# Performance work log

Hardware: AMD Instinct MI355X
Metric: run time of the kernel (lower is better)

## Reference

```python
import jax, jax.numpy as jnp
import numpy as np

# M = batch16 * (128^2+64^2+32^2+16^2+8^2) FPN pixels for 1024x1024 inputs, strides 8..128
M = 349184
C = 80          # num_classes
N_POS = 2048    # positive center locations

ALPHA = 0.25        # hm_focal_alpha
BETA = 4.0          # hm_focal_beta
GAMMA = 2.0         # loss_gamma
SIGMOID_CLAMP = 1e-4
POS_W = 1.0
NEG_W = 1.0
REG_W = 2.0         # reg_weight


def setup_inputs() -> dict:
    key = jax.random.key(0)
    k1, k2, k3, k4, k5, k6 = jax.random.split(key, 6)
    return {
        'logits_pred': jax.random.normal(k1, (M, C), jnp.float32),
        'flattened_hms': jax.random.uniform(k2, (M, C), jnp.float32),
        'reg_pred': jax.random.uniform(k3, (M, 4), jnp.float32),
        'reg_targets': jax.random.normal(k4, (M, 4), jnp.float32),
        'pos_inds': jax.random.randint(k5, (N_POS,), 0, M),
        'labels': jax.random.randint(k6, (N_POS,), 0, C),
    }


def _giou_loss(pred, target):
    # pred/target: [M,4] ltrb distances from grid point to box edges
    pl, pt, pr, pb = pred[:, 0], pred[:, 1], pred[:, 2], pred[:, 3]
    tl, tt, tr, tb = target[:, 0], target[:, 1], target[:, 2], target[:, 3]
    target_area = (tl + tr) * (tt + tb)
    pred_area = (pl + pr) * (pt + pb)
    w_intersect = jnp.minimum(pl, tl) + jnp.minimum(pr, tr)
    h_intersect = jnp.minimum(pb, tb) + jnp.minimum(pt, tt)
    g_w = jnp.maximum(pl, tl) + jnp.maximum(pr, tr)
    g_h = jnp.maximum(pb, tb) + jnp.maximum(pt, tt)
    ac_union = g_w * g_h
    area_intersect = w_intersect * h_intersect
    area_union = target_area + pred_area - area_intersect
    ious = (area_intersect + 1.0) / (area_union + 1.0)
    gious = ious - (ac_union - area_union) / (ac_union + 1e-7)
    return 1.0 - gious  # per-pixel giou loss


def reference(logits_pred, flattened_hms, reg_pred, reg_targets, pos_inds, labels):
    # ---- heatmap focal loss (CenterNet2 heatmap_focal_loss) ----
    pred = jnp.clip(jax.nn.sigmoid(logits_pred), SIGMOID_CLAMP, 1.0 - SIGMOID_CLAMP)
    neg_weights = (1.0 - flattened_hms) ** BETA  # zero at exact positives
    pos_pred = pred[pos_inds, labels]            # irregular gather, [N]
    pos_loss = jnp.log(pos_pred) * (1.0 - pos_pred) ** GAMMA
    neg_loss = jnp.log(1.0 - pred) * pred ** GAMMA * neg_weights
    pos_loss = -ALPHA * jnp.sum(pos_loss)
    neg_loss = -(1.0 - ALPHA) * jnp.sum(neg_loss)
    num_pos_avg = float(max(N_POS, 1))
    pos_loss = POS_W * pos_loss / num_pos_avg
    neg_loss = NEG_W * neg_loss / num_pos_avg

    valid = jnp.max(reg_targets, axis=1) >= 0  # [M] bool, replaces nonzero-gather
    # not_norm_reg=True -> per-location weight 1 on valid rows
    w = valid.astype(reg_pred.dtype)
    safe_targets = jnp.where(valid[:, None], reg_targets, 1.0)
    per_px = _giou_loss(reg_pred, safe_targets)
    reg_norm = jnp.maximum(jnp.sum(w), 1.0)
    reg_loss = REG_W * jnp.sum(per_px * w) / reg_norm

    return jnp.stack([pos_loss, neg_loss, reg_loss])
```

## Files before the change

### kernel.cpp

```cpp
#include <hip/hip_runtime.h>
#include <math.h>

#define M_ROWS   349184
#define C_CH     80
#define NPOS     2048
#define ALPHA    0.25f
#define SIG_CLMP 1.0e-4f
#define REG_W    2.0f

#define NBLOCKS  512
#define NTHREADS 1024
#define N4       6983680
#define CHUNK4   13640
#define ROWS_PB  682
#define POS_PB   4

typedef float vf4 __attribute__((ext_vector_type(4)));

__device__ __forceinline__ float fast_rcp(float x) {
    return __builtin_amdgcn_rcpf(x);
}

__device__ __forceinline__ float clamped_sigmoid(float x) {
    float p = fast_rcp(1.0f + __expf(-x));
    return fminf(fmaxf(p, SIG_CLMP), 1.0f - SIG_CLMP);
}

__device__ __forceinline__ float neg_term(float x, float h) {
    float p = clamped_sigmoid(x);
    float q = 1.0f - h;
    float q2 = q * q;
    return __logf(1.0f - p) * (p * p) * (q2 * q2);
}

__device__ __forceinline__ float neg_term4(vf4 x, vf4 h) {
    return neg_term(x.x, h.x) + neg_term(x.y, h.y) +
           neg_term(x.z, h.z) + neg_term(x.w, h.w);
}

__device__ __forceinline__ vf4 ldnt4(const vf4* p) {
    return __builtin_nontemporal_load(p);
}

__global__ __launch_bounds__(NTHREADS) void centernet_loss_main(
    const float* __restrict__ logits,
    const float* __restrict__ hms,
    const float* __restrict__ reg_pred,
    const float* __restrict__ reg_tgt,
    const int*   __restrict__ pos_inds,
    const int*   __restrict__ labels,
    float4* __restrict__ partials)
{
    const int t = threadIdx.x;
    const int b = ((int)blockIdx.x & 255) * 2 + ((int)blockIdx.x >> 8);

    float neg = 0.0f, giou = 0.0f, wsum = 0.0f, pos = 0.0f;

    const vf4* lg4 = (const vf4*)logits;
    const vf4* hm4 = (const vf4*)hms;

    const int start = b * CHUNK4;
    const int end   = start + CHUNK4;

    int i = start + t;
    for (; i + 5 * NTHREADS < end; i += 6 * NTHREADS) {
        vf4 x0 = ldnt4(&lg4[i]);
        vf4 x1 = ldnt4(&lg4[i + NTHREADS]);
        vf4 x2 = ldnt4(&lg4[i + 2 * NTHREADS]);
        vf4 x3 = ldnt4(&lg4[i + 3 * NTHREADS]);
        vf4 x4 = ldnt4(&lg4[i + 4 * NTHREADS]);
        vf4 x5 = ldnt4(&lg4[i + 5 * NTHREADS]);
        vf4 h0 = ldnt4(&hm4[i]);
        vf4 h1 = ldnt4(&hm4[i + NTHREADS]);
        vf4 h2 = ldnt4(&hm4[i + 2 * NTHREADS]);
        vf4 h3 = ldnt4(&hm4[i + 3 * NTHREADS]);
        vf4 h4 = ldnt4(&hm4[i + 4 * NTHREADS]);
        vf4 h5 = ldnt4(&hm4[i + 5 * NTHREADS]);
        neg += neg_term4(x0, h0);
        neg += neg_term4(x1, h1);
        neg += neg_term4(x2, h2);
        neg += neg_term4(x3, h3);
        neg += neg_term4(x4, h4);
        neg += neg_term4(x5, h5);
    }
    for (; i < end; i += NTHREADS) {
        neg += neg_term4(ldnt4(&lg4[i]), ldnt4(&hm4[i]));
    }

    const int rstart = b * ROWS_PB;
    const vf4* rp4 = (const vf4*)reg_pred;
    const vf4* rt4 = (const vf4*)reg_tgt;
    for (int r = rstart + t; r < rstart + ROWS_PB; r += NTHREADS) {
        vf4 tt = rt4[r];
        float mx = fmaxf(fmaxf(tt.x, tt.y), fmaxf(tt.z, tt.w));
        if (mx >= 0.0f) {
            vf4 p = rp4[r];
            float target_area = (tt.x + tt.z) * (tt.y + tt.w);
            float pred_area   = (p.x + p.z) * (p.y + p.w);
            float w_int = fminf(p.x, tt.x) + fminf(p.z, tt.z);
            float h_int = fminf(p.w, tt.w) + fminf(p.y, tt.y);
            float g_w   = fmaxf(p.x, tt.x) + fmaxf(p.z, tt.z);
            float g_h   = fmaxf(p.w, tt.w) + fmaxf(p.y, tt.y);
            float ac    = g_w * g_h;
            float ai    = w_int * h_int;
            float au    = target_area + pred_area - ai;
            float ious  = (ai + 1.0f) * fast_rcp(au + 1.0f);
            float gious = ious - (ac - au) * fast_rcp(ac + 1e-7f);
            giou += 1.0f - gious;
            wsum += 1.0f;
        }
    }

    if (t < POS_PB) {
        int k = b * POS_PB + t;
        int idx = pos_inds[k] * C_CH + labels[k];
        float p  = clamped_sigmoid(logits[idx]);
        float om = 1.0f - p;
        pos = __logf(p) * om * om;
    }

    const int lane = t & 63;
    const int wave = t >> 6;
    #pragma unroll
    for (int off = 32; off > 0; off >>= 1) {
        neg  += __shfl_down(neg,  off);
        giou += __shfl_down(giou, off);
        wsum += __shfl_down(wsum, off);
        pos  += __shfl_down(pos,  off);
    }
    __shared__ float smem[16][4];
    if (lane == 0) {
        smem[wave][0] = neg;  smem[wave][1] = giou;
        smem[wave][2] = wsum; smem[wave][3] = pos;
    }
    __syncthreads();
    if (t == 0) {
        float4 v = make_float4(0.f, 0.f, 0.f, 0.f);
        #pragma unroll
        for (int w = 0; w < 16; ++w) {
            v.x += smem[w][0]; v.y += smem[w][1];
            v.z += smem[w][2]; v.w += smem[w][3];
        }
        partials[blockIdx.x] = v;
    }
}

__global__ __launch_bounds__(256) void centernet_loss_reduce(
    const float4* __restrict__ partials,
    float* __restrict__ out)
{
    float neg = 0.0f, giou = 0.0f, wsum = 0.0f, pos = 0.0f;
    for (int i = threadIdx.x; i < NBLOCKS; i += 256) {
        float4 v = partials[i];
        neg += v.x; giou += v.y; wsum += v.z; pos += v.w;
    }
    const int lane = threadIdx.x & 63;
    const int wave = threadIdx.x >> 6;
    #pragma unroll
    for (int off = 32; off > 0; off >>= 1) {
        neg  += __shfl_down(neg,  off);
        giou += __shfl_down(giou, off);
        wsum += __shfl_down(wsum, off);
        pos  += __shfl_down(pos,  off);
    }
    __shared__ float smem[4][4];
    if (lane == 0) {
        smem[wave][0] = neg;  smem[wave][1] = giou;
        smem[wave][2] = wsum; smem[wave][3] = pos;
    }
    __syncthreads();
    if (threadIdx.x == 0) {
        float n = smem[0][0] + smem[1][0] + smem[2][0] + smem[3][0];
        float g = smem[0][1] + smem[1][1] + smem[2][1] + smem[3][1];
        float w = smem[0][2] + smem[1][2] + smem[2][2] + smem[3][2];
        float p = smem[0][3] + smem[1][3] + smem[2][3] + smem[3][3];
        const float inv_npos = 1.0f / (float)NPOS;
        out[0] = -ALPHA * p * inv_npos;
        out[1] = -(1.0f - ALPHA) * n * inv_npos;
        out[2] = REG_W * g / fmaxf(w, 1.0f);
    }
}

extern "C" void kernel_launch(void* const* d_in, const int* in_sizes, int n_in,
                              void* d_out, int out_size, void* d_ws, size_t ws_size,
                              hipStream_t stream) {
    const float* logits   = (const float*)d_in[0];
    const float* hms      = (const float*)d_in[1];
    const float* reg_pred = (const float*)d_in[2];
    const float* reg_tgt  = (const float*)d_in[3];
    const int*   pos_inds = (const int*)d_in[4];
    const int*   labels   = (const int*)d_in[5];
    float* out = (float*)d_out;
    float4* partials = (float4*)d_ws;

    centernet_loss_main<<<NBLOCKS, NTHREADS, 0, stream>>>(
        logits, hms, reg_pred, reg_tgt, pos_inds, labels, partials);
    centernet_loss_reduce<<<1, 256, 0, stream>>>(partials, out);
}
```

Before: 234.1 us.

## Drop sigmoid clamp via softplus form, retune grid, use plain loads

Computes the negative focal term as -softplus(x)*sigmoid(x)^2 (and the positive term as -softplus(-x)*(1-p)^2), removing the sigmoid clamp and the divide-then-log path. Doubles the block count with half the threads per block, adds an occupancy hint to launch bounds, and swaps nontemporal loads for ordinary loads issued in interleaved logits/heatmap order. Removing the clamp changes results slightly for extreme logits, and __expf(x) can overflow for large positive x, though the logits are standard normal. The kernel is memory-bound, so the arithmetic savings may not matter much.

```diff
diff --git a/kernel.cpp b/kernel.cpp
--- a/kernel.cpp
+++ b/kernel.cpp
@@ -5,15 +5,14 @@
 #define C_CH     80
 #define NPOS     2048
 #define ALPHA    0.25f
-#define SIG_CLMP 1.0e-4f
 #define REG_W    2.0f
 
-#define NBLOCKS  512
-#define NTHREADS 1024
+#define NBLOCKS  1024
+#define NTHREADS 512
 #define N4       6983680
-#define CHUNK4   13640
-#define ROWS_PB  682
-#define POS_PB   4
+#define CHUNK4   6820
+#define ROWS_PB  341
+#define POS_PB   2
 
 typedef float vf4 __attribute__((ext_vector_type(4)));
 
@@ -21,16 +20,15 @@
     return __builtin_amdgcn_rcpf(x);
 }
 
-__device__ __forceinline__ float clamped_sigmoid(float x) {
-    float p = fast_rcp(1.0f + __expf(-x));
-    return fminf(fmaxf(p, SIG_CLMP), 1.0f - SIG_CLMP);
-}
-
 __device__ __forceinline__ float neg_term(float x, float h) {
-    float p = clamped_sigmoid(x);
-    float q = 1.0f - h;
+    float t  = __expf(x);
+    float u  = 1.0f + t;
+    float L  = __logf(u);
+    float s  = fast_rcp(u);
+    float p  = 1.0f - s;
+    float q  = 1.0f - h;
     float q2 = q * q;
-    return __logf(1.0f - p) * (p * p) * (q2 * q2);
+    return -(L * (p * p) * (q2 * q2));
 }
 
 __device__ __forceinline__ float neg_term4(vf4 x, vf4 h) {
@@ -38,11 +36,7 @@
            neg_term(x.z, h.z) + neg_term(x.w, h.w);
 }
 
-__device__ __forceinline__ vf4 ldnt4(const vf4* p) {
-    return __builtin_nontemporal_load(p);
-}
-
-__global__ __launch_bounds__(NTHREADS) void centernet_loss_main(
+__global__ __launch_bounds__(NTHREADS, 7) void centernet_loss_main(
     const float* __restrict__ logits,
     const float* __restrict__ hms,
     const float* __restrict__ reg_pred,
@@ -52,7 +46,7 @@
     float4* __restrict__ partials)
 {
     const int t = threadIdx.x;
-    const int b = ((int)blockIdx.x & 255) * 2 + ((int)blockIdx.x >> 8);
+    const int b = ((int)blockIdx.x & 255) * 4 + ((int)blockIdx.x >> 8);
 
     float neg = 0.0f, giou = 0.0f, wsum = 0.0f, pos = 0.0f;
 
@@ -64,18 +58,18 @@
 
     int i = start + t;
     for (; i + 5 * NTHREADS < end; i += 6 * NTHREADS) {
-        vf4 x0 = ldnt4(&lg4[i]);
-        vf4 x1 = ldnt4(&lg4[i + NTHREADS]);
-        vf4 x2 = ldnt4(&lg4[i + 2 * NTHREADS]);
-        vf4 x3 = ldnt4(&lg4[i + 3 * NTHREADS]);
-        vf4 x4 = ldnt4(&lg4[i + 4 * NTHREADS]);
-        vf4 x5 = ldnt4(&lg4[i + 5 * NTHREADS]);
-        vf4 h0 = ldnt4(&hm4[i]);
-        vf4 h1 = ldnt4(&hm4[i + NTHREADS]);
-        vf4 h2 = ldnt4(&hm4[i + 2 * NTHREADS]);
-        vf4 h3 = ldnt4(&hm4[i + 3 * NTHREADS]);
-        vf4 h4 = ldnt4(&hm4[i + 4 * NTHREADS]);
-        vf4 h5 = ldnt4(&hm4[i + 5 * NTHREADS]);
+        vf4 x0 = lg4[i];
+        vf4 h0 = hm4[i];
+        vf4 x1 = lg4[i + NTHREADS];
+        vf4 h1 = hm4[i + NTHREADS];
+        vf4 x2 = lg4[i + 2 * NTHREADS];
+        vf4 h2 = hm4[i + 2 * NTHREADS];
+        vf4 x3 = lg4[i + 3 * NTHREADS];
+        vf4 h3 = hm4[i + 3 * NTHREADS];
+        vf4 x4 = lg4[i + 4 * NTHREADS];
+        vf4 h4 = hm4[i + 4 * NTHREADS];
+        vf4 x5 = lg4[i + 5 * NTHREADS];
+        vf4 h5 = hm4[i + 5 * NTHREADS];
         neg += neg_term4(x0, h0);
         neg += neg_term4(x1, h1);
         neg += neg_term4(x2, h2);
@@ -84,7 +78,7 @@
         neg += neg_term4(x5, h5);
     }
     for (; i < end; i += NTHREADS) {
-        neg += neg_term4(ldnt4(&lg4[i]), ldnt4(&hm4[i]));
+        neg += neg_term4(lg4[i], hm4[i]);
     }
 
     const int rstart = b * ROWS_PB;
@@ -114,9 +108,12 @@
     if (t < POS_PB) {
         int k = b * POS_PB + t;
         int idx = pos_inds[k] * C_CH + labels[k];
-        float p  = clamped_sigmoid(logits[idx]);
-        float om = 1.0f - p;
-        pos = __logf(p) * om * om;
+        float x  = logits[idx];
+        float tt = __expf(-x);
+        float u  = 1.0f + tt;
+        float L  = __logf(u);
+        float om = tt * fast_rcp(u);
+        pos = -(L * om * om);
     }
 
     const int lane = t & 63;
@@ -128,7 +125,7 @@
         wsum += __shfl_down(wsum, off);
         pos  += __shfl_down(pos,  off);
     }
-    __shared__ float smem[16][4];
+    __shared__ float smem[8][4];
     if (lane == 0) {
         smem[wave][0] = neg;  smem[wave][1] = giou;
         smem[wave][2] = wsum; smem[wave][3] = pos;
@@ -137,7 +134,7 @@
     if (t == 0) {
         float4 v = make_float4(0.f, 0.f, 0.f, 0.f);
         #pragma unroll
-        for (int w = 0; w < 16; ++w) {
+        for (int w = 0; w < 8; ++w) {
             v.x += smem[w][0]; v.y += smem[w][1];
             v.z += smem[w][2]; v.w += smem[w][3];
         }
```

Result: slower. 255.7 us (+9.2%).
